# Kernel optimization log

Measured on AMD Instinct MI355X. Metric: run time of the kernel, lower is better.

## Reference

```python
import jax, jax.numpy as jnp
import numpy as np

N, H, S, D = 2, 8, 2048, 64

def setup_inputs() -> dict:
    key = jax.random.key(0)
    k1, k2, k3, k4 = jax.random.split(key, 4)
    queries = jax.random.normal(k1, (N, H, S, D), dtype=jnp.float32)
    keys = jax.random.normal(k2, (N, H, S, D), dtype=jnp.float32)
    values = jax.random.normal(k3, (N, H, S, D), dtype=jnp.float32)
    attn_mask = jax.random.randint(k4, (1, 1, S, S), 0, 2, dtype=jnp.int32)
    return {"queries": queries, "keys": keys, "values": values, "attn_mask": attn_mask}

def reference(queries, keys, values, attn_mask):
    # Faithful to the torch code: softmax over axis=2 (query/seq axis) for Q,
    # softmax over axis=1 (heads axis) for K, exactly as written.
    Q = jax.nn.softmax(queries, axis=2)
    K = jax.nn.softmax(keys, axis=1)
    attention_weights = jnp.einsum('nhqd,nhkd->nhqk', Q, K)  # [N,H,S,S]
    attention_weights = jnp.where(attn_mask == 0, -jnp.inf, attention_weights)
    attention_weights = jax.nn.softmax(attention_weights, axis=-1)
    context = jnp.einsum('nhqk,nhkd->nhqd', attention_weights, values)
    return context, attention_weights
```

## Files before the change

kernel.cpp:

```cpp
#include <hip/hip_runtime.h>

#define S 2048
#define Dh 64
#define NH 16
#define SD (S*Dh)
#define SSZ ((size_t)S*(size_t)S)

typedef __attribute__((ext_vector_type(4))) float f32x4;
typedef __attribute__((ext_vector_type(8))) short s16x8;

#define WSB_QSUM 0
#define WSB_RINV 4096
#define WSB_MASK 135168
#define WSB_QS   659456
#define WSB_KS   (WSB_QS + 4194304)
#define WSB_VT   (WSB_KS + 4194304)

__device__ __forceinline__ ushort f2bf(float x) {
    unsigned u = __builtin_bit_cast(unsigned, x);
    u = (u + 0x7fffu + ((u >> 16) & 1u)) >> 16;
    return (ushort)u;
}

__global__ void k_qsum(const float* __restrict__ q, float* __restrict__ qsum) {
    const int head  = blockIdx.x >> 5;
    const int chunk = blockIdx.x & 31;
    const int t = threadIdx.x;
    const int d = t & 63, sg = t >> 6;
    const float* qh = q + (size_t)head * SD;
    const int s0 = chunk * 64;
    float acc = 0.f;
#pragma unroll
    for (int i = 0; i < 16; ++i) {
        int s = s0 + sg + 4 * i;
        acc += __expf(qh[s * Dh + d]);
    }
    __shared__ float part[4][64];
    part[sg][d] = acc;
    __syncthreads();
    if (sg == 0)
        atomicAdd(&qsum[head * 64 + d], part[0][d] + part[1][d] + part[2][d] + part[3][d]);
}

__global__ void k_qnorm(const float* __restrict__ q, const float* __restrict__ qsum,
                        ushort* __restrict__ Qs) {
    const int gid = blockIdx.x * 256 + threadIdx.x;
    const int i0 = gid * 8;
    const int head = i0 >> 17;
    const int d0 = i0 & 63;
    const float4 a = ((const float4*)(q + i0))[0];
    const float4 b = ((const float4*)(q + i0))[1];
    const float* qs = qsum + head * 64 + d0;
    s16x8 o;
    o[0] = (short)f2bf(__expf(a.x) / qs[0]);
    o[1] = (short)f2bf(__expf(a.y) / qs[1]);
    o[2] = (short)f2bf(__expf(a.z) / qs[2]);
    o[3] = (short)f2bf(__expf(a.w) / qs[3]);
    o[4] = (short)f2bf(__expf(b.x) / qs[4]);
    o[5] = (short)f2bf(__expf(b.y) / qs[5]);
    o[6] = (short)f2bf(__expf(b.z) / qs[6]);
    o[7] = (short)f2bf(__expf(b.w) / qs[7]);
    *(s16x8*)(Qs + i0) = o;
}

__global__ void k_ksoft(const float* __restrict__ kin, ushort* __restrict__ Ks) {
    const int gid = blockIdx.x * 256 + threadIdx.x;
    const int n = gid >> 17;
    const int rem = gid & (SD - 1);
    const float* base = kin + (size_t)n * 8 * SD + rem;
    float x[8];
    float sum = 0.f;
#pragma unroll
    for (int h = 0; h < 8; ++h) { x[h] = __expf(base[(size_t)h * SD]); sum += x[h]; }
    const float inv = 1.f / sum;
    ushort* ob = Ks + (size_t)n * 8 * SD + rem;
#pragma unroll
    for (int h = 0; h < 8; ++h) ob[(size_t)h * SD] = f2bf(x[h] * inv);
}

__global__ void k_vt(const float* __restrict__ V, ushort* __restrict__ Vt) {
    const int head = blockIdx.x >> 5, kt = blockIdx.x & 31;
    const int t = threadIdx.x;
    __shared__ float sv[64 * 68];
    const float4* src = (const float4*)(V + (size_t)head * SD + (size_t)kt * 64 * 64);
#pragma unroll
    for (int i = 0; i < 4; ++i) {
        int idx = t + 256 * i;
        int row = idx >> 4, c4 = idx & 15;
        *(float4*)&sv[row * 68 + c4 * 4] = src[idx];
    }
    __syncthreads();
    const int d = t >> 2, seg = t & 3;
    s16x8 v0, v1;
#pragma unroll
    for (int j = 0; j < 8; ++j) v0[j] = (short)f2bf(sv[(seg * 16 + j) * 68 + d]);
#pragma unroll
    for (int j = 0; j < 8; ++j) v1[j] = (short)f2bf(sv[(seg * 16 + 8 + j) * 68 + d]);
    ushort* dst = Vt + (size_t)head * SD + (size_t)d * S + kt * 64 + seg * 16;
    *(s16x8*)dst = v0;
    *(s16x8*)(dst + 8) = v1;
}

__global__ void k_mask(const int* __restrict__ mask, unsigned long long* __restrict__ bm) {
    const int t = threadIdx.x;
    const int g = blockIdx.x * 4 + (t >> 6);
    const int lane = t & 63;
#pragma unroll
    for (int it = 0; it < 16; ++it) {
        int w = g * 16 + it;
        int m = mask[(size_t)w * 64 + lane];
        unsigned long long b = __ballot(m != 0);
        if (lane == 0) bm[w] = b;
    }
}

#define LB 72
#define LF 68

__global__ __launch_bounds__(256, 4) void k_ctx(
        const ushort* __restrict__ Qs, const ushort* __restrict__ Ks,
        const ushort* __restrict__ Vt, const unsigned long long* __restrict__ bm,
        float* __restrict__ ctx, float* __restrict__ rinv) {
    const int head = blockIdx.x, qt = blockIdx.y;
    const int q0 = qt * 32;
    const int t = threadIdx.x;
    const int lane = t & 63, wv = t >> 6;
    const int lm = lane & 15, lg = lane >> 4;
    const int wm = wv & 1;
    const int wn = wv >> 1;

    __shared__ __align__(16) char smem[28416];
    ushort* sQ = (ushort*)smem;
    ushort* sK = (ushort*)(smem + 4608);
    ushort* sV = (ushort*)(smem + 13824);
    ushort* sP = (ushort*)(smem + 23040);
    unsigned long long* sM = (unsigned long long*)(smem + 27648);
    float* sRS = (float*)(smem + 27904);

    {
        const s16x8* src = (const s16x8*)(Qs + (size_t)head * SD + (size_t)q0 * 64);
        int row = t >> 3, seg = t & 7;
        *(s16x8*)&sQ[row * LB + seg * 8] = src[t];
    }

    f32x4 o[2];
    o[0] = (f32x4){0.f, 0.f, 0.f, 0.f};
    o[1] = (f32x4){0.f, 0.f, 0.f, 0.f};
    float rs[4] = {0.f, 0.f, 0.f, 0.f};

    const ushort* Kbase = Ks + (size_t)head * SD;
    const ushort* Vbase = Vt + (size_t)head * SD;

    for (int kt = 0; kt < 32; ++kt) {
        const int k0 = kt * 64;
        __syncthreads();
#pragma unroll
        for (int i = 0; i < 2; ++i) {
            int idx = t + 256 * i;
            int row = idx >> 3, seg = idx & 7;
            *(s16x8*)&sK[row * LB + seg * 8] = *(const s16x8*)(Kbase + (size_t)(k0 + row) * 64 + seg * 8);
            *(s16x8*)&sV[row * LB + seg * 8] = *(const s16x8*)(Vbase + (size_t)row * S + k0 + seg * 8);
        }
        if (t < 32) sM[t] = bm[(size_t)(q0 + t) * 32 + kt];
        __syncthreads();

        f32x4 sc[2];
        sc[0] = (f32x4){0.f, 0.f, 0.f, 0.f};
        sc[1] = (f32x4){0.f, 0.f, 0.f, 0.f};
#pragma unroll
        for (int h = 0; h < 2; ++h) {
            s16x8 aq = *(const s16x8*)&sQ[(16 * wm + lm) * LB + 32 * h + 8 * lg];
#pragma unroll
            for (int j = 0; j < 2; ++j) {
                s16x8 bk = *(const s16x8*)&sK[(16 * (2 * wn + j) + lm) * LB + 32 * h + 8 * lg];
                sc[j] = __builtin_amdgcn_mfma_f32_16x16x32_bf16(aq, bk, sc[j], 0, 0, 0);
            }
        }
#pragma unroll
        for (int r = 0; r < 4; ++r) {
            const int rowl = 16 * wm + 4 * lg + r;
            const unsigned long long m64 = sM[rowl];
            float rsum = 0.f;
#pragma unroll
            for (int j = 0; j < 2; ++j) {
                const int col = 16 * (2 * wn + j) + lm;
                float p = ((m64 >> col) & 1ULL) ? __expf(sc[j][r]) : 0.f;
                rsum += p;
                sP[rowl * LB + col] = f2bf(p);
            }
            rsum += __shfl_xor(rsum, 1);
            rsum += __shfl_xor(rsum, 2);
            rsum += __shfl_xor(rsum, 4);
            rsum += __shfl_xor(rsum, 8);
            rs[r] += rsum;
        }
        __syncthreads();

#pragma unroll
        for (int h = 0; h < 2; ++h) {
            s16x8 ap = *(const s16x8*)&sP[(16 * wm + lm) * LB + 32 * h + 8 * lg];
#pragma unroll
            for (int j = 0; j < 2; ++j) {
                s16x8 bv = *(const s16x8*)&sV[(16 * (2 * wn + j) + lm) * LB + 32 * h + 8 * lg];
                o[j] = __builtin_amdgcn_mfma_f32_16x16x32_bf16(ap, bv, o[j], 0, 0, 0);
            }
        }
    }

    if (lm == 0) {
#pragma unroll
        for (int r = 0; r < 4; ++r)
            sRS[(16 * wm + 4 * lg + r) * 2 + wn] = rs[r];
    }
    __syncthreads();
    if (t < 32) {
        float inv = 1.f / (sRS[t * 2] + sRS[t * 2 + 1]);
        rinv[head * S + q0 + t] = inv;
        sRS[t * 2] = inv;
    }
    __syncthreads();

#pragma unroll
    for (int r = 0; r < 4; ++r) {
        const int rowl = 16 * wm + 4 * lg + r;
        const float inv = sRS[rowl * 2];
        float* cb = ctx + (size_t)head * SD + (size_t)(q0 + rowl) * 64;
#pragma unroll
        for (int j = 0; j < 2; ++j)
            cb[16 * (2 * wn + j) + lm] = o[j][r] * inv;
    }
}

__global__ __launch_bounds__(256, 4) void k_awrite(
        const ushort* __restrict__ Qs, const ushort* __restrict__ Ks,
        const unsigned long long* __restrict__ bm, const float* __restrict__ rinv,
        float* __restrict__ A) {
    const int head = blockIdx.x, qt = blockIdx.y, kc = blockIdx.z;
    const int q0 = qt * 64;
    const int t = threadIdx.x;
    const int lane = t & 63, wv = t >> 6;
    const int lm = lane & 15, lg = lane >> 4;

    __shared__ __align__(16) char smem[36608];
    ushort* sQ = (ushort*)smem;
    ushort* sK = (ushort*)(smem + 9216);
    float* sPf = (float*)(smem + 18432);
    unsigned long long* sM = (unsigned long long*)(smem + 35840);
    float* sI = (float*)(smem + 36352);

    {
        const s16x8* src = (const s16x8*)(Qs + (size_t)head * SD + (size_t)q0 * 64);
#pragma unroll
        for (int i = 0; i < 2; ++i) {
            int idx = t + 256 * i;
            int row = idx >> 3, seg = idx & 7;
            *(s16x8*)&sQ[row * LB + seg * 8] = src[idx];
        }
        if (t < 64) sI[t] = rinv[head * S + q0 + t];
    }

    const ushort* Kbase = Ks + (size_t)head * SD;
    float* Abase = A + (size_t)head * SSZ;

    for (int kt8 = 0; kt8 < 8; ++kt8) {
        const int k0 = kc * 512 + kt8 * 64;
        __syncthreads();
#pragma unroll
        for (int i = 0; i < 2; ++i) {
            int idx = t + 256 * i;
            int row = idx >> 3, seg = idx & 7;
            *(s16x8*)&sK[row * LB + seg * 8] = *(const s16x8*)(Kbase + (size_t)(k0 + row) * 64 + seg * 8);
        }
        if (t < 64) sM[t] = bm[(size_t)(q0 + t) * 32 + (k0 >> 6)];
        __syncthreads();

        f32x4 sc[4];
#pragma unroll
        for (int c = 0; c < 4; ++c) sc[c] = (f32x4){0.f, 0.f, 0.f, 0.f};
#pragma unroll
        for (int h = 0; h < 2; ++h) {
            s16x8 aq = *(const s16x8*)&sQ[(16 * wv + lm) * LB + 32 * h + 8 * lg];
#pragma unroll
            for (int c = 0; c < 4; ++c) {
                s16x8 bk = *(const s16x8*)&sK[(16 * c + lm) * LB + 32 * h + 8 * lg];
                sc[c] = __builtin_amdgcn_mfma_f32_16x16x32_bf16(aq, bk, sc[c], 0, 0, 0);
            }
        }
#pragma unroll
        for (int r = 0; r < 4; ++r) {
            const int rowl = 16 * wv + 4 * lg + r;
            const unsigned long long m64 = sM[rowl];
            const float invr = sI[rowl];
#pragma unroll
            for (int c = 0; c < 4; ++c) {
                const int col = 16 * c + lm;
                sPf[rowl * LF + col] = ((m64 >> col) & 1ULL) ? __expf(sc[c][r]) * invr : 0.f;
            }
        }
        __syncthreads();
#pragma unroll
        for (int i = 0; i < 4; ++i) {
            int idx = t + 256 * i;
            int row = idx >> 4, c4 = idx & 15;
            __builtin_nontemporal_store(
                *(const f32x4*)&sPf[row * LF + c4 * 4],
                (f32x4*)&Abase[(size_t)(q0 + row) * S + k0 + c4 * 4]);
        }
    }
}

extern "C" void kernel_launch(void* const* d_in, const int* in_sizes, int n_in,
                              void* d_out, int out_size, void* d_ws, size_t ws_size,
                              hipStream_t stream) {
    const float* q = (const float*)d_in[0];
    const float* k = (const float*)d_in[1];
    const float* v = (const float*)d_in[2];
    const int* mask = (const int*)d_in[3];
    float* out = (float*)d_out;
    char* ws = (char*)d_ws;

    float* qsum = (float*)(ws + WSB_QSUM);
    float* rinv = (float*)(ws + WSB_RINV);
    unsigned long long* bm = (unsigned long long*)(ws + WSB_MASK);
    ushort* Qs = (ushort*)(ws + WSB_QS);
    ushort* Ks = (ushort*)(ws + WSB_KS);
    ushort* Vt = (ushort*)(ws + WSB_VT);

    (void)hipMemsetAsync(d_ws, 0, 4096, stream);
    k_qsum<<<512, 256, 0, stream>>>(q, qsum);
    k_mask<<<1024, 256, 0, stream>>>(mask, bm);
    k_qnorm<<<1024, 256, 0, stream>>>(q, qsum, Qs);
    k_ksoft<<<1024, 256, 0, stream>>>(k, Ks);
    k_vt<<<512, 256, 0, stream>>>(v, Vt);
    k_ctx<<<dim3(16, 64), 256, 0, stream>>>(Qs, Ks, Vt, bm, out, rinv);
    k_awrite<<<dim3(16, 32, 4), 256, 0, stream>>>(Qs, Ks, bm, rinv, out + (size_t)NH * SD);
}
```

Baseline: 407.8 us.

## Compute transposed score tiles in registers, drop shared K/V staging and barriers

Result: slower. 494.3 us (+21.2%).

```diff
diff --git a/kernel.cpp b/kernel.cpp
--- a/kernel.cpp
+++ b/kernel.cpp
@@ -101,7 +101,7 @@
     *(s16x8*)(dst + 8) = v1;
 }
 
-__global__ void k_mask(const int* __restrict__ mask, unsigned long long* __restrict__ bm) {
+__global__ void k_mask(const int* __restrict__ mask, unsigned long long* __restrict__ bmt) {
     const int t = threadIdx.x;
     const int g = blockIdx.x * 4 + (t >> 6);
     const int lane = t & 63;
@@ -110,201 +110,153 @@
         int w = g * 16 + it;
         int m = mask[(size_t)w * 64 + lane];
         unsigned long long b = __ballot(m != 0);
-        if (lane == 0) bm[w] = b;
-    }
-}
-
-#define LB 72
-#define LF 68
+        if (lane == 0) bmt[(size_t)(w & 31) * S + (w >> 5)] = b;
+    }
+}
 
 __global__ __launch_bounds__(256, 4) void k_ctx(
         const ushort* __restrict__ Qs, const ushort* __restrict__ Ks,
-        const ushort* __restrict__ Vt, const unsigned long long* __restrict__ bm,
+        const ushort* __restrict__ Vt, const unsigned long long* __restrict__ bmt,
         float* __restrict__ ctx, float* __restrict__ rinv) {
     const int head = blockIdx.x, qt = blockIdx.y;
     const int q0 = qt * 32;
     const int t = threadIdx.x;
-    const int lane = t & 63, wv = t >> 6;
+    const int lane = t & 63, w = t >> 6;
+    const int wq = w & 1, par = w >> 1;
     const int lm = lane & 15, lg = lane >> 4;
-    const int wm = wv & 1;
-    const int wn = wv >> 1;
-
-    __shared__ __align__(16) char smem[28416];
-    ushort* sQ = (ushort*)smem;
-    ushort* sK = (ushort*)(smem + 4608);
-    ushort* sV = (ushort*)(smem + 13824);
-    ushort* sP = (ushort*)(smem + 23040);
-    unsigned long long* sM = (unsigned long long*)(smem + 27648);
-    float* sRS = (float*)(smem + 27904);
-
-    {
-        const s16x8* src = (const s16x8*)(Qs + (size_t)head * SD + (size_t)q0 * 64);
-        int row = t >> 3, seg = t & 7;
-        *(s16x8*)&sQ[row * LB + seg * 8] = src[t];
-    }
-
-    f32x4 o[2];
-    o[0] = (f32x4){0.f, 0.f, 0.f, 0.f};
-    o[1] = (f32x4){0.f, 0.f, 0.f, 0.f};
-    float rs[4] = {0.f, 0.f, 0.f, 0.f};
-
-    const ushort* Kbase = Ks + (size_t)head * SD;
-    const ushort* Vbase = Vt + (size_t)head * SD;
-
-    for (int kt = 0; kt < 32; ++kt) {
+    const int q = q0 + 16 * wq + lm;
+
+    __shared__ __align__(16) ushort Pl[4][16][72];
+    __shared__ __align__(16) float redo[2][64][20];
+    __shared__ float redrs[2][16];
+
+    const ushort* Qb = Qs + (size_t)head * SD;
+    const ushort* Kb = Ks + (size_t)head * SD;
+    const ushort* Vb = Vt + (size_t)head * SD;
+
+    s16x8 bq[2];
+#pragma unroll
+    for (int h = 0; h < 2; ++h)
+        bq[h] = *(const s16x8*)(Qb + (size_t)q * 64 + 32 * h + 8 * lg);
+
+    const ushort* kr[4];
+    const ushort* vr[4];
+#pragma unroll
+    for (int j = 0; j < 4; ++j) kr[j] = Kb + (size_t)(16 * j + lm) * 64 + 8 * lg;
+#pragma unroll
+    for (int dj = 0; dj < 4; ++dj) vr[dj] = Vb + (size_t)(16 * dj + lm) * S + 8 * lg;
+
+    f32x4 o[4];
+#pragma unroll
+    for (int dj = 0; dj < 4; ++dj) o[dj] = (f32x4){0.f, 0.f, 0.f, 0.f};
+    float rs = 0.f;
+    uint* prow = (uint*)&Pl[w][lm][0];
+
+    for (int kt = par; kt < 32; kt += 2) {
         const int k0 = kt * 64;
-        __syncthreads();
-#pragma unroll
-        for (int i = 0; i < 2; ++i) {
-            int idx = t + 256 * i;
-            int row = idx >> 3, seg = idx & 7;
-            *(s16x8*)&sK[row * LB + seg * 8] = *(const s16x8*)(Kbase + (size_t)(k0 + row) * 64 + seg * 8);
-            *(s16x8*)&sV[row * LB + seg * 8] = *(const s16x8*)(Vbase + (size_t)row * S + k0 + seg * 8);
+        f32x4 sc[4];
+#pragma unroll
+        for (int j = 0; j < 4; ++j) sc[j] = (f32x4){0.f, 0.f, 0.f, 0.f};
+#pragma unroll
+        for (int h = 0; h < 2; ++h)
+#pragma unroll
+            for (int j = 0; j < 4; ++j) {
+                s16x8 ak = *(const s16x8*)(kr[j] + (size_t)k0 * 64 + 32 * h);
+                sc[j] = __builtin_amdgcn_mfma_f32_16x16x32_bf16(ak, bq[h], sc[j], 0, 0, 0);
+            }
+        const unsigned long long m64 = bmt[(size_t)kt * S + q];
+        float rsum = 0.f;
+#pragma unroll
+        for (int j = 0; j < 4; ++j)
+#pragma unroll
+            for (int p = 0; p < 2; ++p) {
+                const int b0 = 16 * j + 4 * lg + 2 * p;
+                const float e0 = ((m64 >> b0) & 1ULL) ? __expf(sc[j][2 * p]) : 0.f;
+                const float e1 = ((m64 >> (b0 + 1)) & 1ULL) ? __expf(sc[j][2 * p + 1]) : 0.f;
+                rsum += e0 + e1;
+                prow[8 * j + 2 * lg + p] = ((uint)f2bf(e1) << 16) | (uint)f2bf(e0);
+            }
+        rsum += __shfl_xor(rsum, 16);
+        rsum += __shfl_xor(rsum, 32);
+        rs += rsum;
+#pragma unroll
+        for (int c = 0; c < 2; ++c) {
+            const s16x8 pb = *(const s16x8*)&Pl[w][lm][32 * c + 8 * lg];
+#pragma unroll
+            for (int dj = 0; dj < 4; ++dj) {
+                s16x8 av = *(const s16x8*)(vr[dj] + k0 + 32 * c);
+                o[dj] = __builtin_amdgcn_mfma_f32_16x16x32_bf16(av, pb, o[dj], 0, 0, 0);
+            }
         }
-        if (t < 32) sM[t] = bm[(size_t)(q0 + t) * 32 + kt];
-        __syncthreads();
-
-        f32x4 sc[2];
-        sc[0] = (f32x4){0.f, 0.f, 0.f, 0.f};
-        sc[1] = (f32x4){0.f, 0.f, 0.f, 0.f};
-#pragma unroll
-        for (int h = 0; h < 2; ++h) {
-            s16x8 aq = *(const s16x8*)&sQ[(16 * wm + lm) * LB + 32 * h + 8 * lg];
-#pragma unroll
-            for (int j = 0; j < 2; ++j) {
-                s16x8 bk = *(const s16x8*)&sK[(16 * (2 * wn + j) + lm) * LB + 32 * h + 8 * lg];
-                sc[j] = __builtin_amdgcn_mfma_f32_16x16x32_bf16(aq, bk, sc[j], 0, 0, 0);
-            }
+    }
+
+    if (par == 1) {
+        float* dst = &redo[wq][lane][0];
+#pragma unroll
+        for (int dj = 0; dj < 4; ++dj) *(f32x4*)&dst[dj * 4] = o[dj];
+        if (lg == 0) redrs[wq][lm] = rs;
+    }
+    __syncthreads();
+    if (par == 0) {
+        const float inv = 1.f / (rs + redrs[wq][lm]);
+        if (lg == 0) rinv[head * S + q] = inv;
+        const float* src = &redo[wq][lane][0];
+        float* cb = ctx + (size_t)head * SD + (size_t)q * 64;
+#pragma unroll
+        for (int dj = 0; dj < 4; ++dj) {
+            f32x4 oo = (o[dj] + *(const f32x4*)&src[dj * 4]) * inv;
+            *(f32x4*)(cb + 16 * dj + 4 * lg) = oo;
         }
-#pragma unroll
-        for (int r = 0; r < 4; ++r) {
-            const int rowl = 16 * wm + 4 * lg + r;
-            const unsigned long long m64 = sM[rowl];
-            float rsum = 0.f;
-#pragma unroll
-            for (int j = 0; j < 2; ++j) {
-                const int col = 16 * (2 * wn + j) + lm;
-                float p = ((m64 >> col) & 1ULL) ? __expf(sc[j][r]) : 0.f;
-                rsum += p;
-                sP[rowl * LB + col] = f2bf(p);
-            }
-            rsum += __shfl_xor(rsum, 1);
-            rsum += __shfl_xor(rsum, 2);
-            rsum += __shfl_xor(rsum, 4);
-            rsum += __shfl_xor(rsum, 8);
-            rs[r] += rsum;
-        }
-        __syncthreads();
-
-#pragma unroll
-        for (int h = 0; h < 2; ++h) {
-            s16x8 ap = *(const s16x8*)&sP[(16 * wm + lm) * LB + 32 * h + 8 * lg];
-#pragma unroll
-            for (int j = 0; j < 2; ++j) {
-                s16x8 bv = *(const s16x8*)&sV[(16 * (2 * wn + j) + lm) * LB + 32 * h + 8 * lg];
-                o[j] = __builtin_amdgcn_mfma_f32_16x16x32_bf16(ap, bv, o[j], 0, 0, 0);
-            }
-        }
-    }
-
-    if (lm == 0) {
-#pragma unroll
-        for (int r = 0; r < 4; ++r)
-            sRS[(16 * wm + 4 * lg + r) * 2 + wn] = rs[r];
-    }
-    __syncthreads();
-    if (t < 32) {
-        float inv = 1.f / (sRS[t * 2] + sRS[t * 2 + 1]);
-        rinv[head * S + q0 + t] = inv;
-        sRS[t * 2] = inv;
-    }
-    __syncthreads();
-
-#pragma unroll
-    for (int r = 0; r < 4; ++r) {
-        const int rowl = 16 * wm + 4 * lg + r;
-        const float inv = sRS[rowl * 2];
-        float* cb = ctx + (size_t)head * SD + (size_t)(q0 + rowl) * 64;
-#pragma unroll
-        for (int j = 0; j < 2; ++j)
-            cb[16 * (2 * wn + j) + lm] = o[j][r] * inv;
     }
 }
 
 __global__ __launch_bounds__(256, 4) void k_awrite(
         const ushort* __restrict__ Qs, const ushort* __restrict__ Ks,
-        const unsigned long long* __restrict__ bm, const float* __restrict__ rinv,
+        const unsigned long long* __restrict__ bmt, const float* __restrict__ rinv,
         float* __restrict__ A) {
     const int head = blockIdx.x, qt = blockIdx.y, kc = blockIdx.z;
     const int q0 = qt * 64;
     const int t = threadIdx.x;
     const int lane = t & 63, wv = t >> 6;
     const int lm = lane & 15, lg = lane >> 4;
-
-    __shared__ __align__(16) char smem[36608];
-    ushort* sQ = (ushort*)smem;
-    ushort* sK = (ushort*)(smem + 9216);
-    float* sPf = (float*)(smem + 18432);
-    unsigned long long* sM = (unsigned long long*)(smem + 35840);
-    float* sI = (float*)(smem + 36352);
-
-    {
-        const s16x8* src = (const s16x8*)(Qs + (size_t)head * SD + (size_t)q0 * 64);
-#pragma unroll
-        for (int i = 0; i < 2; ++i) {
-            int idx = t + 256 * i;
-            int row = idx >> 3, seg = idx & 7;
-            *(s16x8*)&sQ[row * LB + seg * 8] = src[idx];
-        }
-        if (t < 64) sI[t] = rinv[head * S + q0 + t];
-    }
-
-    const ushort* Kbase = Ks + (size_t)head * SD;
-    float* Abase = A + (size_t)head * SSZ;
+    const int q = q0 + 16 * wv + lm;
+
+    const ushort* Qb = Qs + (size_t)head * SD;
+    const ushort* Kb = Ks + (size_t)head * SD;
+    float* Abase = A + (size_t)head * SSZ + (size_t)q * S;
+
+    s16x8 bq[2];
+#pragma unroll
+    for (int h = 0; h < 2; ++h)
+        bq[h] = *(const s16x8*)(Qb + (size_t)q * 64 + 32 * h + 8 * lg);
+    const float invr = rinv[head * S + q];
+
+    const ushort* kr[4];
+#pragma unroll
+    for (int j = 0; j < 4; ++j) kr[j] = Kb + (size_t)(16 * j + lm) * 64 + 8 * lg;
 
     for (int kt8 = 0; kt8 < 8; ++kt8) {
         const int k0 = kc * 512 + kt8 * 64;
-        __syncthreads();
-#pragma unroll
-        for (int i = 0; i < 2; ++i) {
-            int idx = t + 256 * i;
-            int row = idx >> 3, seg = idx & 7;
-            *(s16x8*)&sK[row * LB + seg * 8] = *(const s16x8*)(Kbase + (size_t)(k0 + row) * 64 + seg * 8);
-        }
-        if (t < 64) sM[t] = bm[(size_t)(q0 + t) * 32 + (k0 >> 6)];
-        __syncthreads();
-
         f32x4 sc[4];
 #pragma unroll
-        for (int c = 0; c < 4; ++c) sc[c] = (f32x4){0.f, 0.f, 0.f, 0.f};
-#pragma unroll
-        for (int h = 0; h < 2; ++h) {
-            s16x8 aq = *(const s16x8*)&sQ[(16 * wv + lm) * LB + 32 * h + 8 * lg];
-#pragma unroll
-            for (int c = 0; c < 4; ++c) {
-                s16x8 bk = *(const s16x8*)&sK[(16 * c + lm) * LB + 32 * h + 8 * lg];
-                sc[c] = __builtin_amdgcn_mfma_f32_16x16x32_bf16(aq, bk, sc[c], 0, 0, 0);
-            }
-        }
-#pragma unroll
-        for (int r = 0; r < 4; ++r) {
-            const int rowl = 16 * wv + 4 * lg + r;
-            const unsigned long long m64 = sM[rowl];
-            const float invr = sI[rowl];
-#pragma unroll
-            for (int c = 0; c < 4; ++c) {
-                const int col = 16 * c + lm;
-                sPf[rowl * LF + col] = ((m64 >> col) & 1ULL) ? __expf(sc[c][r]) * invr : 0.f;
-            }
-        }
-        __syncthreads();
-#pragma unroll
-        for (int i = 0; i < 4; ++i) {
-            int idx = t + 256 * i;
-            int row = idx >> 4, c4 = idx & 15;
-            __builtin_nontemporal_store(
-                *(const f32x4*)&sPf[row * LF + c4 * 4],
-                (f32x4*)&Abase[(size_t)(q0 + row) * S + k0 + c4 * 4]);
+        for (int j = 0; j < 4; ++j) sc[j] = (f32x4){0.f, 0.f, 0.f, 0.f};
+#pragma unroll
+        for (int h = 0; h < 2; ++h)
+#pragma unroll
+            for (int j = 0; j < 4; ++j) {
+                s16x8 ak = *(const s16x8*)(kr[j] + (size_t)k0 * 64 + 32 * h);
+                sc[j] = __builtin_amdgcn_mfma_f32_16x16x32_bf16(ak, bq[h], sc[j], 0, 0, 0);
+            }
+        const unsigned long long m64 = bmt[(size_t)(k0 >> 6) * S + q];
+#pragma unroll
+        for (int j = 0; j < 4; ++j) {
+            f32x4 pv;
+#pragma unroll
+            for (int r = 0; r < 4; ++r) {
+                const int b = 16 * j + 4 * lg + r;
+                pv[r] = ((m64 >> b) & 1ULL) ? __expf(sc[j][r]) * invr : 0.f;
+            }
+            __builtin_nontemporal_store(pv, (f32x4*)&Abase[k0 + 16 * j + 4 * lg]);
         }
     }
 }
```
